# Kernel tuning notes

Measured on AMD Instinct MI355X. Metric: run time of the kernel, lower is better.

## Reference

```python
import jax, jax.numpy as jnp
import numpy as np

N_NODES = 100000
N_EDGES = 800000
N_GRAPHS = 2000
IN_DIM = 64
HID = 32
HEADS = 4
NEG_SLOPE = 0.2


def _glorot(key, shape, fan_in, fan_out):
    lim = np.sqrt(6.0 / (fan_in + fan_out)).astype(np.float32)
    return jax.random.uniform(key, shape, jnp.float32, -lim, lim)


def setup_inputs() -> dict:
    key = jax.random.key(0)
    ks = jax.random.split(key, 16)
    x = jax.random.normal(ks[0], (N_NODES, IN_DIM), jnp.float32)
    edge_index = jax.random.randint(ks[1], (2, N_EDGES), 0, N_NODES, jnp.int64)
    batch = jnp.sort(jax.random.randint(ks[2], (N_NODES,), 0, N_GRAPHS, jnp.int64))
    HF = HEADS * HID
    params = {
        "W1": _glorot(ks[3], (IN_DIM, HF), IN_DIM, HF),
        "a1_src": _glorot(ks[4], (HEADS, HID), HID, HID),
        "a1_dst": _glorot(ks[5], (HEADS, HID), HID, HID),
        "b1": jnp.zeros((HF,), jnp.float32),
        "W2": _glorot(ks[6], (HF, HF), HF, HF),
        "a2_src": _glorot(ks[7], (HEADS, HID), HID, HID),
        "a2_dst": _glorot(ks[8], (HEADS, HID), HID, HID),
        "b2": jnp.zeros((HF,), jnp.float32),
        "W3": _glorot(ks[9], (HF, HF), HF, HF),
        "a3_src": _glorot(ks[10], (HEADS, HID), HID, HID),
        "a3_dst": _glorot(ks[11], (HEADS, HID), HID, HID),
        "b3": jnp.zeros((HID,), jnp.float32),  # concat=False -> bias over out dim
        "Wm1": _glorot(ks[12], (HID, 64), HID, 64),
        "bm1": jnp.zeros((64,), jnp.float32),
        "Wm2": _glorot(ks[13], (64, 1), 64, 1),
        "bm2": jnp.zeros((1,), jnp.float32),
    }
    return {"x": x, "edge_index": edge_index, "batch": batch, **params}


def gat_conv(x, src, dst, W, a_src, a_dst, bias, concat):
    # PyG GATConv (eval mode, self-loops already in src/dst).
    N = x.shape[0]
    H, F = a_src.shape
    h = (x @ W).reshape(N, H, F)                     # [N,H,F]
    as_n = jnp.sum(h * a_src, axis=-1)               # [N,H] per-node src term
    ad_n = jnp.sum(h * a_dst, axis=-1)               # [N,H] per-node dst term
    logits = jax.nn.leaky_relu(as_n[src] + ad_n[dst], NEG_SLOPE)  # [Et,H]
    # segment softmax over incoming edges of each dst node
    m = jax.ops.segment_max(logits, dst, num_segments=N)          # [N,H]
    e = jnp.exp(logits - m[dst])
    denom = jax.ops.segment_sum(e, dst, num_segments=N)           # [N,H], >0 via self-loops
    alpha = e / denom[dst]                                        # [Et,H]
    msg = h[src] * alpha[:, :, None]                              # [Et,H,F]
    out = jax.ops.segment_sum(msg, dst, num_segments=N)           # [N,H,F]
    out = out.reshape(N, H * F) if concat else out.mean(axis=1)
    return out + bias


def reference(x, edge_index, batch, W1, a1_src, a1_dst, b1, W2, a2_src, a2_dst, b2,
              W3, a3_src, a3_dst, b3, Wm1, bm1, Wm2, bm2):
    N = x.shape[0]
    loops = jnp.arange(N, dtype=edge_index.dtype)
    src = jnp.concatenate([edge_index[0], loops])
    dst = jnp.concatenate([edge_index[1], loops])

    h = jax.nn.elu(gat_conv(x, src, dst, W1, a1_src, a1_dst, b1, True))
    h = jax.nn.elu(gat_conv(h, src, dst, W2, a2_src, a2_dst, b2, True))
    h = jax.nn.elu(gat_conv(h, src, dst, W3, a3_src, a3_dst, b3, False))

    # global_mean_pool over batch ids
    sums = jax.ops.segment_sum(h, batch, num_segments=N_GRAPHS)           # [G,HID]
    cnts = jax.ops.segment_sum(jnp.ones((N,), h.dtype), batch, num_segments=N_GRAPHS)
    pooled = sums / jnp.maximum(cnts, 1.0)[:, None]

    z = jax.nn.relu(pooled @ Wm1 + bm1)
    out = (z @ Wm2 + bm2).squeeze(-1)                                     # [G]
    return out
```

## Files before the change

### kernel.cpp

```cpp
#include <hip/hip_runtime.h>

#define N_NODES  100000
#define N_EDGES  800000
#define ET       900000
#define N_GRAPHS 2000
#define IN_DIM   64
#define HID      32
#define HEADS    4
#define HF       128
#define NEG_SLOPE 0.2f

__device__ __forceinline__ float lrelu(float x) { return x > 0.f ? x : NEG_SLOPE * x; }
__device__ __forceinline__ float elu_f(float x) { return x > 0.f ? x : expm1f(x); }
__device__ __forceinline__ unsigned fenc(float f) {
  unsigned u = __float_as_uint(f);
  return (u & 0x80000000u) ? ~u : (u | 0x80000000u);
}
__device__ __forceinline__ float fdec(unsigned e) {
  return __uint_as_float((e & 0x80000000u) ? (e ^ 0x80000000u) : ~e);
}

__global__ void k_count(const int* __restrict__ ei, int* __restrict__ deg) {
  int e = blockIdx.x * 256 + threadIdx.x;
  if (e >= ET) return;
  int d = (e < N_EDGES) ? ei[N_EDGES + e] : (e - N_EDGES);
  atomicAdd(&deg[d], 1);
}

__global__ void k_scan1(const int* __restrict__ deg, int* __restrict__ rs, int* __restrict__ bsums) {
  __shared__ int sd[256];
  int t = threadIdx.x;
  int i = blockIdx.x * 256 + t;
  int v = (i < N_NODES) ? deg[i] : 0;
  sd[t] = v; __syncthreads();
  for (int s = 1; s < 256; s <<= 1) {
    int tmp = (t >= s) ? sd[t - s] : 0; __syncthreads();
    sd[t] += tmp; __syncthreads();
  }
  if (i < N_NODES) rs[i] = sd[t] - v;
  if (t == 255) bsums[blockIdx.x] = sd[255];
}

__global__ void k_scan2(int* __restrict__ bsums, int nb) {
  __shared__ int sd[512];
  int t = threadIdx.x;
  int v = (t < nb) ? bsums[t] : 0;
  sd[t] = v; __syncthreads();
  for (int s = 1; s < 512; s <<= 1) {
    int tmp = (t >= s) ? sd[t - s] : 0; __syncthreads();
    sd[t] += tmp; __syncthreads();
  }
  if (t < nb) bsums[t] = sd[t] - v;
}

__global__ void k_scan3(int* __restrict__ rs, const int* __restrict__ bsums) {
  int i = blockIdx.x * 256 + threadIdx.x;
  if (i < N_NODES) rs[i] += bsums[blockIdx.x];
  if (i == 0) rs[N_NODES] = ET;
}

__global__ void k_fill(const int* __restrict__ ei, const int* __restrict__ rs,
                       int* __restrict__ fill, int* __restrict__ csr_src) {
  int e = blockIdx.x * 256 + threadIdx.x;
  if (e >= ET) return;
  int s, d;
  if (e < N_EDGES) { s = ei[e]; d = ei[N_EDGES + e]; }
  else             { s = e - N_EDGES; d = s; }
  int pos = atomicAdd(&fill[d], 1);
  csr_src[rs[d] + pos] = s;
}

#define XRS 132
#define WRS 144
__device__ __forceinline__ int wofs(int c) { return c + 4 * (c >> 5); }

template<int K>
__global__ void __launch_bounds__(256, 4) k_gemm_attn(
    const float* __restrict__ X, const float* __restrict__ Wg,
    const float* __restrict__ av_src, const float* __restrict__ av_dst,
    float* __restrict__ H, float* __restrict__ AS, float* __restrict__ AD,
    unsigned* __restrict__ M4) {
  __shared__ float sXT[32 * XRS];
  __shared__ float sW[32 * WRS];
  __shared__ unsigned smax[HEADS];
  const int t = threadIdx.x;
  const int tr = t >> 4;
  const int tc = t & 15;
  const int r0 = tr * 8;
  const int c0 = tc * 8;
  const int head = tc >> 2;
  const int quar = tc & 3;
  const int row0 = blockIdx.x * 128;
  const int wbase = wofs(c0);

  if (t < HEADS) smax[t] = 0;

  float acc[8][8];
#pragma unroll
  for (int i = 0; i < 8; ++i)
#pragma unroll
    for (int j = 0; j < 8; ++j) acc[i][j] = 0.f;

  for (int kb = 0; kb < K; kb += 32) {
    __syncthreads();
    for (int i = t; i < 128 * 32; i += 256) {
      int kc = i & 31, r = i >> 5;
      int gr = row0 + r;
      sXT[kc * XRS + r] = (gr < N_NODES) ? X[(size_t)gr * K + kb + kc] : 0.f;
    }
    for (int i = t; i < 32 * 128; i += 256) {
      int k2 = i >> 7, c = i & 127;
      sW[k2 * WRS + wofs(c)] = Wg[(size_t)(kb + k2) * HF + c];
    }
    __syncthreads();
#pragma unroll 8
    for (int k2 = 0; k2 < 32; ++k2) {
      float4 x0 = *(const float4*)&sXT[k2 * XRS + r0];
      float4 x1 = *(const float4*)&sXT[k2 * XRS + r0 + 4];
      float4 w0 = *(const float4*)&sW[k2 * WRS + wbase];
      float4 w1 = *(const float4*)&sW[k2 * WRS + wbase + 4];
      float xv[8] = {x0.x, x0.y, x0.z, x0.w, x1.x, x1.y, x1.z, x1.w};
      float wv[8] = {w0.x, w0.y, w0.z, w0.w, w1.x, w1.y, w1.z, w1.w};
#pragma unroll
      for (int i = 0; i < 8; ++i)
#pragma unroll
        for (int j = 0; j < 8; ++j) acc[i][j] += xv[i] * wv[j];
    }
  }

  float aS[8], aD[8];
#pragma unroll
  for (int j = 0; j < 8; ++j) {
    aS[j] = av_src[head * HID + quar * 8 + j];
    aD[j] = av_dst[head * HID + quar * 8 + j];
  }
  float pdS[8], pdD[8];
#pragma unroll
  for (int i = 0; i < 8; ++i) {
    float s = 0.f, d = 0.f;
#pragma unroll
    for (int j = 0; j < 8; ++j) { s += acc[i][j] * aS[j]; d += acc[i][j] * aD[j]; }
    pdS[i] = s; pdD[i] = d;
  }
#pragma unroll
  for (int i = 0; i < 8; ++i) {
    pdS[i] += __shfl_xor(pdS[i], 1);  pdD[i] += __shfl_xor(pdD[i], 1);
    pdS[i] += __shfl_xor(pdS[i], 2);  pdD[i] += __shfl_xor(pdD[i], 2);
  }

  float mloc = -3.4e38f;
#pragma unroll
  for (int i = 0; i < 8; ++i) {
    int gr = row0 + r0 + i;
    if (gr < N_NODES) {
      float4* hrow = (float4*)&H[(size_t)gr * HF + c0];
      hrow[0] = make_float4(acc[i][0], acc[i][1], acc[i][2], acc[i][3]);
      hrow[1] = make_float4(acc[i][4], acc[i][5], acc[i][6], acc[i][7]);
      if (quar == 0) {
        AS[gr * HEADS + head] = pdS[i];
        AD[gr * HEADS + head] = pdD[i];
        mloc = fmaxf(mloc, pdS[i]);
      }
    }
  }
  if (quar == 0) atomicMax(&smax[head], fenc(mloc));
  __syncthreads();
  if (t < HEADS) atomicMax(&M4[t], smax[t]);
}

template<bool CONCAT>
__global__ void __launch_bounds__(256) k_aggregate(
    const int* __restrict__ rs, const int* __restrict__ csr_src,
    const float* __restrict__ H, const float* __restrict__ AS,
    const float* __restrict__ AD, const unsigned* __restrict__ M4,
    const float* __restrict__ bias, float* __restrict__ OUT) {
  int n = blockIdx.x * 8 + (threadIdx.x >> 5);
  if (n >= N_NODES) return;
  int sl = threadIdx.x & 31;
  int c = sl * 4;
  int head = sl >> 3;
  int b = rs[n], e = rs[n + 1];

  float ad = AD[4 * n + head];
  float m = lrelu(fdec(M4[head]) + ad);

  float ax = 0.f, ay = 0.f, az = 0.f, aw = 0.f, den = 0.f;
  int jj = b;
  for (; jj + 3 < e; jj += 4) {
    int s0 = csr_src[jj];
    int s1 = csr_src[jj + 1];
    int s2 = csr_src[jj + 2];
    int s3 = csr_src[jj + 3];
    float e0 = __expf(lrelu(AS[4 * s0 + head] + ad) - m);
    float e1 = __expf(lrelu(AS[4 * s1 + head] + ad) - m);
    float e2 = __expf(lrelu(AS[4 * s2 + head] + ad) - m);
    float e3 = __expf(lrelu(AS[4 * s3 + head] + ad) - m);
    float4 h0 = *(const float4*)&H[(size_t)s0 * HF + c];
    float4 h1 = *(const float4*)&H[(size_t)s1 * HF + c];
    float4 h2 = *(const float4*)&H[(size_t)s2 * HF + c];
    float4 h3 = *(const float4*)&H[(size_t)s3 * HF + c];
    ax += h0.x * e0 + h1.x * e1 + h2.x * e2 + h3.x * e3;
    ay += h0.y * e0 + h1.y * e1 + h2.y * e2 + h3.y * e3;
    az += h0.z * e0 + h1.z * e1 + h2.z * e2 + h3.z * e3;
    aw += h0.w * e0 + h1.w * e1 + h2.w * e2 + h3.w * e3;
    den += (e0 + e1) + (e2 + e3);
  }
  for (; jj < e; ++jj) {
    int s0 = csr_src[jj];
    float e0 = __expf(lrelu(AS[4 * s0 + head] + ad) - m);
    float4 h0 = *(const float4*)&H[(size_t)s0 * HF + c];
    ax += h0.x * e0; ay += h0.y * e0; az += h0.z * e0; aw += h0.w * e0;
    den += e0;
  }

  float invd = 1.f / den;
  if (CONCAT) {
    float4 o;
    o.x = elu_f(ax * invd + bias[c]);
    o.y = elu_f(ay * invd + bias[c + 1]);
    o.z = elu_f(az * invd + bias[c + 2]);
    o.w = elu_f(aw * invd + bias[c + 3]);
    *(float4*)&OUT[(size_t)n * HF + c] = o;
  } else {
    ax *= invd; ay *= invd; az *= invd; aw *= invd;
    ax += __shfl_xor(ax, 8);  ay += __shfl_xor(ay, 8);
    az += __shfl_xor(az, 8);  aw += __shfl_xor(aw, 8);
    ax += __shfl_xor(ax, 16); ay += __shfl_xor(ay, 16);
    az += __shfl_xor(az, 16); aw += __shfl_xor(aw, 16);
    if (sl < 8) {
      int cc = sl * 4;
      float4 o;
      o.x = elu_f(0.25f * ax + bias[cc]);
      o.y = elu_f(0.25f * ay + bias[cc + 1]);
      o.z = elu_f(0.25f * az + bias[cc + 2]);
      o.w = elu_f(0.25f * aw + bias[cc + 3]);
      *(float4*)&OUT[(size_t)n * HID + cc] = o;
    }
  }
}

__global__ void __launch_bounds__(64) k_pool_mlp(
    const int* __restrict__ batch, const float* __restrict__ H3,
    const float* __restrict__ Wm1, const float* __restrict__ bm1,
    const float* __restrict__ Wm2, const float* __restrict__ bm2,
    float* __restrict__ OUT) {
  int g = blockIdx.x;
  int t = threadIdx.x;
  __shared__ float pooled[HID];
  int lo = 0, hi = N_NODES;
  while (lo < hi) { int mid = (lo + hi) >> 1; if (batch[mid] < g) lo = mid + 1; else hi = mid; }
  int start = lo;
  hi = N_NODES;
  while (lo < hi) { int mid = (lo + hi) >> 1; if (batch[mid] < g + 1) lo = mid + 1; else hi = mid; }
  int end = lo;
  if (t < HID) {
    float s = 0.f;
    for (int n = start; n < end; ++n) s += H3[(size_t)n * HID + t];
    float cnt = (float)(end - start);
    pooled[t] = s / fmaxf(cnt, 1.f);
  }
  __syncthreads();
  float z = bm1[t];
#pragma unroll
  for (int f = 0; f < HID; ++f) z += pooled[f] * Wm1[f * 64 + t];
  z = fmaxf(z, 0.f);
  float p = z * Wm2[t];
  for (int off = 32; off > 0; off >>= 1) p += __shfl_down(p, off);
  if (t == 0) OUT[g] = p + bm2[0];
}

extern "C" void kernel_launch(void* const* d_in, const int* in_sizes, int n_in,
                              void* d_out, int out_size, void* d_ws, size_t ws_size,
                              hipStream_t stream) {
  const float* x    = (const float*)d_in[0];
  const int*   ei   = (const int*)d_in[1];
  const int*   batch= (const int*)d_in[2];
  const float* W1   = (const float*)d_in[3];
  const float* a1s  = (const float*)d_in[4];
  const float* a1d  = (const float*)d_in[5];
  const float* b1   = (const float*)d_in[6];
  const float* W2   = (const float*)d_in[7];
  const float* a2s  = (const float*)d_in[8];
  const float* a2d  = (const float*)d_in[9];
  const float* b2   = (const float*)d_in[10];
  const float* W3   = (const float*)d_in[11];
  const float* a3s  = (const float*)d_in[12];
  const float* a3d  = (const float*)d_in[13];
  const float* b3   = (const float*)d_in[14];
  const float* Wm1  = (const float*)d_in[15];
  const float* bm1  = (const float*)d_in[16];
  const float* Wm2  = (const float*)d_in[17];
  const float* bm2  = (const float*)d_in[18];
  float* out = (float*)d_out;

  char* p = (char*)d_ws;
  auto take = [&](size_t bytes) { char* r = p; p += (bytes + 255) & ~(size_t)255; return r; };
  float*    bufA  = (float*)take((size_t)N_NODES * HF * 4);
  float*    bufB  = (float*)take((size_t)N_NODES * HF * 4);
  float*    AS    = (float*)take((size_t)N_NODES * HEADS * 4);
  float*    AD    = (float*)take((size_t)N_NODES * HEADS * 4);
  unsigned* M4    = (unsigned*)take(3 * 4 * 4);
  int*      deg   = (int*)take((size_t)N_NODES * 4);
  int*      rs    = (int*)take((size_t)(N_NODES + 1) * 4);
  int*      csr   = (int*)take((size_t)ET * 4);
  int*      bsums = (int*)take((size_t)512 * 4);

  unsigned* M4a = M4;
  unsigned* M4b = M4 + 4;
  unsigned* M4c = M4 + 8;

  const int nb_scan = (N_NODES + 255) / 256;

  hipMemsetAsync(deg, 0, (size_t)N_NODES * 4, stream);
  hipMemsetAsync(M4, 0, 48, stream);
  k_count<<<(ET + 255) / 256, 256, 0, stream>>>(ei, deg);
  k_scan1<<<nb_scan, 256, 0, stream>>>(deg, rs, bsums);
  k_scan2<<<1, 512, 0, stream>>>(bsums, nb_scan);
  k_scan3<<<nb_scan, 256, 0, stream>>>(rs, bsums);
  hipMemsetAsync(deg, 0, (size_t)N_NODES * 4, stream);
  k_fill<<<(ET + 255) / 256, 256, 0, stream>>>(ei, rs, deg, csr);

  const int gb = (N_NODES + 127) / 128;
  const int ab = (N_NODES + 7) / 8;

  k_gemm_attn<IN_DIM><<<gb, 256, 0, stream>>>(x, W1, a1s, a1d, bufA, AS, AD, M4a);
  k_aggregate<true><<<ab, 256, 0, stream>>>(rs, csr, bufA, AS, AD, M4a, b1, bufB);
  k_gemm_attn<HF><<<gb, 256, 0, stream>>>(bufB, W2, a2s, a2d, bufA, AS, AD, M4b);
  k_aggregate<true><<<ab, 256, 0, stream>>>(rs, csr, bufA, AS, AD, M4b, b2, bufB);
  k_gemm_attn<HF><<<gb, 256, 0, stream>>>(bufB, W3, a3s, a3d, bufA, AS, AD, M4c);
  k_aggregate<false><<<ab, 256, 0, stream>>>(rs, csr, bufA, AS, AD, M4c, b3, bufB);
  k_pool_mlp<<<N_GRAPHS, 64, 0, stream>>>(batch, bufB, Wm1, bm1, Wm2, bm2, out);
}
```

Baseline: 548.9 us.

## Prefetch next GEMM k-tile into registers with vectorized float4 global loads

The GEMM+attention kernel now loads each 32-wide k-tile of X and W into registers as float4 vectors and prefetches the next tile while the current one is computed from shared memory. This replaces the scalar per-element global loads and aims to overlap global latency with FMA work. The extra 32 prefetch registers lead to lowering the launch-bounds occupancy hint from 4 to 3 blocks per SM, which may reduce latency hiding elsewhere.

```diff
diff --git a/kernel.cpp b/kernel.cpp
--- a/kernel.cpp
+++ b/kernel.cpp
@@ -75,7 +75,7 @@
 __device__ __forceinline__ int wofs(int c) { return c + 4 * (c >> 5); }
 
 template<int K>
-__global__ void __launch_bounds__(256, 4) k_gemm_attn(
+__global__ void __launch_bounds__(256, 3) k_gemm_attn(
     const float* __restrict__ X, const float* __restrict__ Wg,
     const float* __restrict__ av_src, const float* __restrict__ av_dst,
     float* __restrict__ H, float* __restrict__ AS, float* __restrict__ AD,
@@ -95,23 +95,48 @@
 
   if (t < HEADS) smax[t] = 0;
 
+  const int xr = t >> 3;
+  const int xk = (t & 7) * 4;
+  const int wk = t >> 5;
+  const int wc = (t & 31) * 4;
+  const int wdst = wofs(wc);
+
+  float4 xreg[4], wreg[4];
+#define LOADREGS(kb)                                                           \
+  {                                                                            \
+    _Pragma("unroll")                                                          \
+    for (int p = 0; p < 4; ++p) {                                              \
+      int gr = row0 + xr + 32 * p;                                             \
+      xreg[p] = (gr < N_NODES)                                                 \
+          ? *(const float4*)&X[(size_t)gr * K + (kb) + xk]                     \
+          : make_float4(0.f, 0.f, 0.f, 0.f);                                   \
+      wreg[p] = *(const float4*)&Wg[(size_t)((kb) + wk + 8 * p) * HF + wc];    \
+    }                                                                          \
+  }
+#define STOREREGS()                                                            \
+  {                                                                            \
+    _Pragma("unroll")                                                          \
+    for (int p = 0; p < 4; ++p) {                                              \
+      int rr = xr + 32 * p;                                                    \
+      sXT[(xk + 0) * XRS + rr] = xreg[p].x;                                    \
+      sXT[(xk + 1) * XRS + rr] = xreg[p].y;                                    \
+      sXT[(xk + 2) * XRS + rr] = xreg[p].z;                                    \
+      sXT[(xk + 3) * XRS + rr] = xreg[p].w;                                    \
+      *(float4*)&sW[(wk + 8 * p) * WRS + wdst] = wreg[p];                      \
+    }                                                                          \
+  }
+
   float acc[8][8];
 #pragma unroll
   for (int i = 0; i < 8; ++i)
 #pragma unroll
     for (int j = 0; j < 8; ++j) acc[i][j] = 0.f;
 
+  LOADREGS(0);
   for (int kb = 0; kb < K; kb += 32) {
     __syncthreads();
-    for (int i = t; i < 128 * 32; i += 256) {
-      int kc = i & 31, r = i >> 5;
-      int gr = row0 + r;
-      sXT[kc * XRS + r] = (gr < N_NODES) ? X[(size_t)gr * K + kb + kc] : 0.f;
-    }
-    for (int i = t; i < 32 * 128; i += 256) {
-      int k2 = i >> 7, c = i & 127;
-      sW[k2 * WRS + wofs(c)] = Wg[(size_t)(kb + k2) * HF + c];
-    }
+    STOREREGS();
+    if (kb + 32 < K) LOADREGS(kb + 32);
     __syncthreads();
 #pragma unroll 8
     for (int k2 = 0; k2 < 32; ++k2) {
@@ -127,6 +152,8 @@
         for (int j = 0; j < 8; ++j) acc[i][j] += xv[i] * wv[j];
     }
   }
+#undef LOADREGS
+#undef STOREREGS
 
   float aS[8], aD[8];
 #pragma unroll
```

Result: faster. 527.4 us (-3.9%).

## Use split-bf16 MFMA for GAT projection GEMMs with folded attention vectors

Applied to the files above, without the earlier changes.

Replaces the FP32 shared-memory register-tiled GEMM with bf16 MFMA 16x16x32 instructions, using a hi/lo bf16 split (three MFMAs per tile) to keep near-FP32 accuracy. A prep kernel packs the weights into an MFMA-friendly layout and appends 8 extra columns holding W·a_src and W·a_dst per head, so the attention scalars come out of the same matmul instead of a separate dot-product epilogue. X is loaded directly from global memory without LDS staging. The costs are three MFMAs per product, three extra small prep launches, and scalar (non-vectorized) H stores.

```diff
diff --git a/kernel.cpp b/kernel.cpp
--- a/kernel.cpp
+++ b/kernel.cpp
@@ -10,6 +10,9 @@
 #define HF       128
 #define NEG_SLOPE 0.2f
 
+typedef __attribute__((ext_vector_type(8))) short bf16x8;
+typedef __attribute__((ext_vector_type(4))) float f32x4;
+
 __device__ __forceinline__ float lrelu(float x) { return x > 0.f ? x : NEG_SLOPE * x; }
 __device__ __forceinline__ float elu_f(float x) { return x > 0.f ? x : expm1f(x); }
 __device__ __forceinline__ unsigned fenc(float f) {
@@ -18,6 +21,11 @@
 }
 __device__ __forceinline__ float fdec(unsigned e) {
   return __uint_as_float((e & 0x80000000u) ? (e ^ 0x80000000u) : ~e);
+}
+__device__ __forceinline__ unsigned short bf16_rne(float f) {
+  unsigned u = __float_as_uint(f);
+  unsigned r = (u + 0x7fffu + ((u >> 16) & 1u)) >> 16;
+  return (unsigned short)r;
 }
 
 __global__ void k_count(const int* __restrict__ ei, int* __restrict__ deg) {
@@ -70,102 +78,111 @@
   csr_src[rs[d] + pos] = s;
 }
 
-#define XRS 132
-#define WRS 144
-__device__ __forceinline__ int wofs(int c) { return c + 4 * (c >> 5); }
-
 template<int K>
-__global__ void __launch_bounds__(256, 4) k_gemm_attn(
-    const float* __restrict__ X, const float* __restrict__ Wg,
-    const float* __restrict__ av_src, const float* __restrict__ av_dst,
+__global__ void k_prep(const float* __restrict__ W, const float* __restrict__ as_,
+                       const float* __restrict__ ad_,
+                       unsigned short* __restrict__ Bh, unsigned short* __restrict__ Bl) {
+  int idx = blockIdx.x * 256 + threadIdx.x;
+  if (idx >= K * 144) return;
+  int k = idx / 144, c = idx % 144;
+  float v = 0.f;
+  if (c < 128) {
+    v = W[k * 128 + c];
+  } else if (c < 136) {
+    int h = (c - 128) & 3;
+    const float* av = (c < 132) ? as_ : ad_;
+    float s = 0.f;
+    for (int f = 0; f < HID; ++f) s += W[k * 128 + h * HID + f] * av[h * HID + f];
+    v = s;
+  }
+  unsigned short hi = bf16_rne(v);
+  float hf = __uint_as_float((unsigned)hi << 16);
+  unsigned short lo = bf16_rne(v - hf);
+  size_t dst = ((size_t)(k >> 3) * 144 + c) * 8 + (k & 7);
+  Bh[dst] = hi;
+  Bl[dst] = lo;
+}
+
+template<int K>
+__global__ void __launch_bounds__(256, 3) k_gemm_attn(
+    const float* __restrict__ X,
+    const unsigned short* __restrict__ Bh, const unsigned short* __restrict__ Bl,
     float* __restrict__ H, float* __restrict__ AS, float* __restrict__ AD,
     unsigned* __restrict__ M4) {
-  __shared__ float sXT[32 * XRS];
-  __shared__ float sW[32 * WRS];
-  __shared__ unsigned smax[HEADS];
-  const int t = threadIdx.x;
-  const int tr = t >> 4;
-  const int tc = t & 15;
-  const int r0 = tr * 8;
-  const int c0 = tc * 8;
-  const int head = tc >> 2;
-  const int quar = tc & 3;
-  const int row0 = blockIdx.x * 128;
-  const int wbase = wofs(c0);
-
-  if (t < HEADS) smax[t] = 0;
-
-  float acc[8][8];
-#pragma unroll
-  for (int i = 0; i < 8; ++i)
-#pragma unroll
-    for (int j = 0; j < 8; ++j) acc[i][j] = 0.f;
+  const int l = threadIdx.x & 63;
+  const int w = threadIdx.x >> 6;
+  const int m = l & 15;
+  const int g = l >> 4;
+  const int row0 = blockIdx.x * 128 + w * 32;
+
+  f32x4 acc[2][9];
+#pragma unroll
+  for (int a = 0; a < 2; ++a)
+#pragma unroll
+    for (int b = 0; b < 9; ++b) acc[a][b] = (f32x4){0.f, 0.f, 0.f, 0.f};
 
   for (int kb = 0; kb < K; kb += 32) {
-    __syncthreads();
-    for (int i = t; i < 128 * 32; i += 256) {
-      int kc = i & 31, r = i >> 5;
-      int gr = row0 + r;
-      sXT[kc * XRS + r] = (gr < N_NODES) ? X[(size_t)gr * K + kb + kc] : 0.f;
-    }
-    for (int i = t; i < 32 * 128; i += 256) {
-      int k2 = i >> 7, c = i & 127;
-      sW[k2 * WRS + wofs(c)] = Wg[(size_t)(kb + k2) * HF + c];
-    }
-    __syncthreads();
-#pragma unroll 8
-    for (int k2 = 0; k2 < 32; ++k2) {
-      float4 x0 = *(const float4*)&sXT[k2 * XRS + r0];
-      float4 x1 = *(const float4*)&sXT[k2 * XRS + r0 + 4];
-      float4 w0 = *(const float4*)&sW[k2 * WRS + wbase];
-      float4 w1 = *(const float4*)&sW[k2 * WRS + wbase + 4];
-      float xv[8] = {x0.x, x0.y, x0.z, x0.w, x1.x, x1.y, x1.z, x1.w};
-      float wv[8] = {w0.x, w0.y, w0.z, w0.w, w1.x, w1.y, w1.z, w1.w};
-#pragma unroll
-      for (int i = 0; i < 8; ++i)
-#pragma unroll
-        for (int j = 0; j < 8; ++j) acc[i][j] += xv[i] * wv[j];
-    }
-  }
-
-  float aS[8], aD[8];
-#pragma unroll
-  for (int j = 0; j < 8; ++j) {
-    aS[j] = av_src[head * HID + quar * 8 + j];
-    aD[j] = av_dst[head * HID + quar * 8 + j];
-  }
-  float pdS[8], pdD[8];
-#pragma unroll
-  for (int i = 0; i < 8; ++i) {
-    float s = 0.f, d = 0.f;
-#pragma unroll
-    for (int j = 0; j < 8; ++j) { s += acc[i][j] * aS[j]; d += acc[i][j] * aD[j]; }
-    pdS[i] = s; pdD[i] = d;
-  }
-#pragma unroll
-  for (int i = 0; i < 8; ++i) {
-    pdS[i] += __shfl_xor(pdS[i], 1);  pdD[i] += __shfl_xor(pdD[i], 1);
-    pdS[i] += __shfl_xor(pdS[i], 2);  pdD[i] += __shfl_xor(pdD[i], 2);
-  }
-
-  float mloc = -3.4e38f;
-#pragma unroll
-  for (int i = 0; i < 8; ++i) {
-    int gr = row0 + r0 + i;
-    if (gr < N_NODES) {
-      float4* hrow = (float4*)&H[(size_t)gr * HF + c0];
-      hrow[0] = make_float4(acc[i][0], acc[i][1], acc[i][2], acc[i][3]);
-      hrow[1] = make_float4(acc[i][4], acc[i][5], acc[i][6], acc[i][7]);
-      if (quar == 0) {
-        AS[gr * HEADS + head] = pdS[i];
-        AD[gr * HEADS + head] = pdD[i];
-        mloc = fmaxf(mloc, pdS[i]);
-      }
-    }
-  }
-  if (quar == 0) atomicMax(&smax[head], fenc(mloc));
-  __syncthreads();
-  if (t < HEADS) atomicMax(&M4[t], smax[t]);
+    bf16x8 ahi[2], alo[2];
+#pragma unroll
+    for (int tr = 0; tr < 2; ++tr) {
+      int row = row0 + tr * 16 + m;
+      float4 xa = make_float4(0.f, 0.f, 0.f, 0.f);
+      float4 xb = make_float4(0.f, 0.f, 0.f, 0.f);
+      if (row < N_NODES) {
+        const float4* xp = (const float4*)&X[(size_t)row * K + kb + g * 8];
+        xa = xp[0]; xb = xp[1];
+      }
+      float xv[8] = {xa.x, xa.y, xa.z, xa.w, xb.x, xb.y, xb.z, xb.w};
+#pragma unroll
+      for (int j = 0; j < 8; ++j) {
+        unsigned short h = bf16_rne(xv[j]);
+        float hf = __uint_as_float((unsigned)h << 16);
+        unsigned short lo2 = bf16_rne(xv[j] - hf);
+        ahi[tr][j] = (short)h;
+        alo[tr][j] = (short)lo2;
+      }
+    }
+    const size_t kf = ((size_t)(kb >> 3) + g) * 144;
+#pragma unroll
+    for (int tc = 0; tc < 9; ++tc) {
+      bf16x8 bh = *(const bf16x8*)(Bh + (kf + tc * 16 + m) * 8);
+      bf16x8 bl = *(const bf16x8*)(Bl + (kf + tc * 16 + m) * 8);
+#pragma unroll
+      for (int tr = 0; tr < 2; ++tr) {
+        acc[tr][tc] = __builtin_amdgcn_mfma_f32_16x16x32_bf16(ahi[tr], bh, acc[tr][tc], 0, 0, 0);
+        acc[tr][tc] = __builtin_amdgcn_mfma_f32_16x16x32_bf16(ahi[tr], bl, acc[tr][tc], 0, 0, 0);
+        acc[tr][tc] = __builtin_amdgcn_mfma_f32_16x16x32_bf16(alo[tr], bh, acc[tr][tc], 0, 0, 0);
+      }
+    }
+  }
+
+  float vmax = -3.4e38f;
+#pragma unroll
+  for (int tr = 0; tr < 2; ++tr) {
+    int rbase = row0 + tr * 16 + g * 4;
+#pragma unroll
+    for (int tc = 0; tc < 8; ++tc) {
+      int col = tc * 16 + m;
+#pragma unroll
+      for (int e = 0; e < 4; ++e) {
+        int row = rbase + e;
+        if (row < N_NODES) H[(size_t)row * HF + col] = acc[tr][tc][e];
+      }
+    }
+#pragma unroll
+    for (int e = 0; e < 4; ++e) {
+      int row = rbase + e;
+      float v = acc[tr][8][e];
+      if (row < N_NODES) {
+        if (m < 4) AS[row * HEADS + m] = v;
+        else if (m < 8) AD[row * HEADS + (m - 4)] = v;
+      }
+      vmax = fmaxf(vmax, v);
+    }
+  }
+  vmax = fmaxf(vmax, __shfl_xor(vmax, 16));
+  vmax = fmaxf(vmax, __shfl_xor(vmax, 32));
+  if (g == 0 && m < 4) atomicMax(&M4[m], fenc(vmax));
 }
 
 template<bool CONCAT>
@@ -295,21 +312,31 @@
 
   char* p = (char*)d_ws;
   auto take = [&](size_t bytes) { char* r = p; p += (bytes + 255) & ~(size_t)255; return r; };
-  float*    bufA  = (float*)take((size_t)N_NODES * HF * 4);
-  float*    bufB  = (float*)take((size_t)N_NODES * HF * 4);
-  float*    AS    = (float*)take((size_t)N_NODES * HEADS * 4);
-  float*    AD    = (float*)take((size_t)N_NODES * HEADS * 4);
-  unsigned* M4    = (unsigned*)take(3 * 4 * 4);
-  int*      deg   = (int*)take((size_t)N_NODES * 4);
-  int*      rs    = (int*)take((size_t)(N_NODES + 1) * 4);
-  int*      csr   = (int*)take((size_t)ET * 4);
-  int*      bsums = (int*)take((size_t)512 * 4);
+  float*          bufA = (float*)take((size_t)N_NODES * HF * 4);
+  float*          bufB = (float*)take((size_t)N_NODES * HF * 4);
+  float*          AS   = (float*)take((size_t)N_NODES * HEADS * 4);
+  float*          AD   = (float*)take((size_t)N_NODES * HEADS * 4);
+  unsigned*       M4   = (unsigned*)take(3 * 4 * 4);
+  int*            deg  = (int*)take((size_t)N_NODES * 4);
+  int*            rs   = (int*)take((size_t)(N_NODES + 1) * 4);
+  int*            csr  = (int*)take((size_t)ET * 4);
+  int*            bsums= (int*)take((size_t)512 * 4);
+  unsigned short* Wh1  = (unsigned short*)take((size_t)IN_DIM * 144 * 2);
+  unsigned short* Wl1  = (unsigned short*)take((size_t)IN_DIM * 144 * 2);
+  unsigned short* Wh2  = (unsigned short*)take((size_t)HF * 144 * 2);
+  unsigned short* Wl2  = (unsigned short*)take((size_t)HF * 144 * 2);
+  unsigned short* Wh3  = (unsigned short*)take((size_t)HF * 144 * 2);
+  unsigned short* Wl3  = (unsigned short*)take((size_t)HF * 144 * 2);
 
   unsigned* M4a = M4;
   unsigned* M4b = M4 + 4;
   unsigned* M4c = M4 + 8;
 
   const int nb_scan = (N_NODES + 255) / 256;
+
+  k_prep<IN_DIM><<<(IN_DIM * 144 + 255) / 256, 256, 0, stream>>>(W1, a1s, a1d, Wh1, Wl1);
+  k_prep<HF><<<(HF * 144 + 255) / 256, 256, 0, stream>>>(W2, a2s, a2d, Wh2, Wl2);
+  k_prep<HF><<<(HF * 144 + 255) / 256, 256, 0, stream>>>(W3, a3s, a3d, Wh3, Wl3);
 
   hipMemsetAsync(deg, 0, (size_t)N_NODES * 4, stream);
   hipMemsetAsync(M4, 0, 48, stream);
@@ -323,11 +350,11 @@
   const int gb = (N_NODES + 127) / 128;
   const int ab = (N_NODES + 7) / 8;
 
-  k_gemm_attn<IN_DIM><<<gb, 256, 0, stream>>>(x, W1, a1s, a1d, bufA, AS, AD, M4a);
+  k_gemm_attn<IN_DIM><<<gb, 256, 0, stream>>>(x, Wh1, Wl1, bufA, AS, AD, M4a);
   k_aggregate<true><<<ab, 256, 0, stream>>>(rs, csr, bufA, AS, AD, M4a, b1, bufB);
-  k_gemm_attn<HF><<<gb, 256, 0, stream>>>(bufB, W2, a2s, a2d, bufA, AS, AD, M4b);
+  k_gemm_attn<HF><<<gb, 256, 0, stream>>>(bufB, Wh2, Wl2, bufA, AS, AD, M4b);
   k_aggregate<true><<<ab, 256, 0, stream>>>(rs, csr, bufA, AS, AD, M4b, b2, bufB);
-  k_gemm_attn<HF><<<gb, 256, 0, stream>>>(bufB, W3, a3s, a3d, bufA, AS, AD, M4c);
+  k_gemm_attn<HF><<<gb, 256, 0, stream>>>(bufB, Wh3, Wl3, bufA, AS, AD, M4c);
   k_aggregate<false><<<ab, 256, 0, stream>>>(rs, csr, bufA, AS, AD, M4c, b3, bufB);
   k_pool_mlp<<<N_GRAPHS, 64, 0, stream>>>(batch, bufB, Wm1, bm1, Wm2, bm2, out);
 }
```

New measurement: 562.0 us. 1.02x slower.
